# Optimization experiments

Hardware: AMD Instinct MI355X
Metric: run time of the kernel (lower is better)

## Reference

```python
import jax, jax.numpy as jnp
import numpy as np

# module hyperparameters (from init_kwargs)
STRIDE, PAD, DIL = 1, 1, 1
GROUPS, DG = 1, 1
KH, KW = 3, 3
CIN, COUT = 256, 256


def _mdcn_forward(x, offset, mask, weight, bias):
    B, C, H, W = x.shape
    Cout = weight.shape[0]
    K = KH * KW
    Ho = (H + 2 * PAD - (DIL * (KH - 1) + 1)) // STRIDE + 1
    Wo = (W + 2 * PAD - (DIL * (KW - 1) + 1)) // STRIDE + 1
    Cg = C // DG

    # offset channel layout: ((g*K + k)*2 + {0: dy, 1: dx})
    off = offset.reshape(B, DG, KH, KW, 2, Ho, Wo)
    base_y = (jnp.arange(Ho) * STRIDE - PAD)[None, :] + DIL * jnp.arange(KH)[:, None]  # [KH,Ho]
    base_x = (jnp.arange(Wo) * STRIDE - PAD)[None, :] + DIL * jnp.arange(KW)[:, None]  # [KW,Wo]
    sy = base_y[None, None, :, None, :, None].astype(x.dtype) + off[:, :, :, :, 0]  # [B,DG,KH,KW,Ho,Wo]
    sx = base_x[None, None, None, :, None, :].astype(x.dtype) + off[:, :, :, :, 1]

    y0f = jnp.floor(sy); x0f = jnp.floor(sx)
    wy = sy - y0f; wx = sx - x0f
    y0 = y0f.astype(jnp.int32); x0 = x0f.astype(jnp.int32)

    xg = x.reshape(B, DG, Cg, H * W)

    def corner(yc, xc, w):
        valid = (yc >= 0) & (yc < H) & (xc >= 0) & (xc < W)
        idx = jnp.clip(yc, 0, H - 1) * W + jnp.clip(xc, 0, W - 1)  # [B,DG,KH,KW,Ho,Wo]
        v = jnp.take_along_axis(xg, idx.reshape(B, DG, 1, -1), axis=3)  # [B,DG,Cg,K*Ho*Wo]
        v = v.reshape(B, DG, Cg, KH, KW, Ho, Wo)
        return v * (w * valid.astype(x.dtype))[:, :, None]

    val = (corner(y0, x0, (1 - wy) * (1 - wx))
           + corner(y0, x0 + 1, (1 - wy) * wx)
           + corner(y0 + 1, x0, wy * (1 - wx))
           + corner(y0 + 1, x0 + 1, wy * wx))  # [B,DG,Cg,KH,KW,Ho,Wo]

    cols = val * mask.reshape(B, DG, 1, KH, KW, Ho, Wo)
    cols = cols.reshape(B, GROUPS, (C // GROUPS) * K, Ho * Wo)
    wg = weight.reshape(GROUPS, Cout // GROUPS, (C // GROUPS) * K)
    out = jnp.einsum('gok,bgkp->bgop', wg, cols).reshape(B, Cout, Ho, Wo)
    return out + bias[None, :, None, None]


def setup_inputs() -> dict:
    key = jax.random.key(0)
    k1, k2, k3, k4 = jax.random.split(key, 4)
    B, H, W = 4, 64, 64
    x = jax.random.normal(k1, (B, CIN, H, W), dtype=jnp.float32)
    offset = jax.random.normal(k2, (B, 2 * DG * KH * KW, H, W), dtype=jnp.float32)
    mask = jax.random.uniform(k3, (B, DG * KH * KW, H, W), dtype=jnp.float32)
    stdv = 1.0 / np.sqrt(CIN * KH * KW)
    weight = jax.random.uniform(k4, (COUT, CIN // GROUPS, KH, KW), dtype=jnp.float32,
                                minval=-stdv, maxval=stdv)
    bias = jnp.zeros((COUT,), dtype=jnp.float32)
    return {"x": x, "offset": offset, "mask": mask, "weight": weight, "bias": bias}


def reference(x, offset, mask, weight, bias):
    return _mdcn_forward(x, offset, mask, weight, bias)
```

## Files before the change

kernel.cpp:

```cpp
#include <hip/hip_runtime.h>
#include <hip/hip_bf16.h>
#include <stdint.h>

#define KDIM 2304

typedef __bf16 bf16_t;
typedef bf16_t bf16x8 __attribute__((ext_vector_type(8)));
typedef float f32x4 __attribute__((ext_vector_type(4)));
typedef float f32x2 __attribute__((ext_vector_type(2)));

__device__ __forceinline__ float b2f_lo(uint32_t u) {
  union { uint32_t i; float f; } c; c.i = u << 16; return c.f;
}
__device__ __forceinline__ float b2f_hi(uint32_t u) {
  union { uint32_t i; float f; } c; c.i = u & 0xffff0000u; return c.f;
}
__device__ __forceinline__ uint32_t pk_bf16(float a, float b) {
  __hip_bfloat162 h = __float22bfloat162_rn(make_float2(a, b));
  union { __hip_bfloat162 h; uint32_t u; } c; c.h = h; return c.u;
}

__device__ __forceinline__ void g2lds16(const uint16_t* g, uint16_t* l) {
  __builtin_amdgcn_global_load_lds((const __attribute__((address_space(1))) void*)g,
                                   (__attribute__((address_space(3))) void*)l,
                                   16, 0, 0);
}

__global__ __launch_bounds__(256) void k_prep(const float* __restrict__ x,
                                              uint16_t* __restrict__ xt,
                                              const float* __restrict__ w,
                                              uint16_t* __restrict__ wt) {
  int tid = threadIdx.x;
  if (blockIdx.x < 2048) {
    __shared__ float tile[32][65];
    int b = blockIdx.x >> 9;
    int cgrp = (blockIdx.x >> 6) & 7;
    int sgrp = blockIdx.x & 63;
    int c0 = cgrp << 5, s0 = sgrp << 6;
#pragma unroll
    for (int it = 0; it < 2; ++it) {
      int f = tid + it * 256;
      int rr = f >> 4, col = (f & 15) << 2;
      float4 v = *(const float4*)&x[((size_t)(b * 256 + c0 + rr)) * 4096 + s0 + col];
      tile[rr][col + 0] = v.x;
      tile[rr][col + 1] = v.y;
      tile[rr][col + 2] = v.z;
      tile[rr][col + 3] = v.w;
    }
    __syncthreads();
    int sp = tid >> 2, cg = tid & 3;
    uint4 o;
    o.x = pk_bf16(tile[cg * 8 + 0][sp], tile[cg * 8 + 1][sp]);
    o.y = pk_bf16(tile[cg * 8 + 2][sp], tile[cg * 8 + 3][sp]);
    o.z = pk_bf16(tile[cg * 8 + 4][sp], tile[cg * 8 + 5][sp]);
    o.w = pk_bf16(tile[cg * 8 + 6][sp], tile[cg * 8 + 7][sp]);
    *(uint4*)&xt[((size_t)b * 4096 + s0 + sp) * 256 + c0 + cg * 8] = o;
  } else {
    __shared__ float wl[2304];
    int cout = blockIdx.x - 2048;
    const float* wrow = w + (size_t)cout * 2304;
    for (int i = tid; i < 576; i += 256)
      *(float4*)&wl[i * 4] = *(const float4*)&wrow[i * 4];
    __syncthreads();
    uint16_t* wdst = wt + (size_t)cout * KDIM + tid;
#pragma unroll
    for (int t = 0; t < 9; ++t)
      wdst[t * 256] = (uint16_t)(pk_bf16(wl[tid * 9 + t], 0.f) & 0xffffu);
  }
}

__device__ __forceinline__ void mk_corners(int tap, int p, int ho,
                                           const float* s_off, const float* s_msk,
                                           const uint16_t* xtb,
                                           float cw[4], const uint16_t* cp[4]) {
  int kh = tap / 3, kw = tap - kh * 3;
  float dy = s_off[(2 * tap) * 64 + p];
  float dx = s_off[(2 * tap + 1) * 64 + p];
  float mm = s_msk[tap * 64 + p];
  float sy = (float)(ho - 1 + kh) + dy;
  float sx = (float)(p - 1 + kw) + dx;
  float fy = floorf(sy), fx = floorf(sx);
  int y0 = (int)fy, x0 = (int)fx;
  float wy = sy - fy, wx = sx - fx;
#pragma unroll
  for (int cy = 0; cy < 2; ++cy) {
#pragma unroll
    for (int cx = 0; cx < 2; ++cx) {
      int y = y0 + cy, xx = x0 + cx;
      float wgt = (cy ? wy : 1.f - wy) * (cx ? wx : 1.f - wx) * mm;
      bool v = ((unsigned)y < 64u) && ((unsigned)xx < 64u);
      wgt = v ? wgt : 0.f;
      int yc = min(max(y, 0), 63), xc = min(max(xx, 0), 63);
      cw[cy * 2 + cx] = wgt;
      cp[cy * 2 + cx] = xtb + ((yc << 6) + xc) * 256;
    }
  }
}

__device__ __forceinline__ uint4 blend4(const uint4 d[4], const float cw[4]) {
  f32x2 f0 = {0.f, 0.f}, f1 = {0.f, 0.f}, f2 = {0.f, 0.f}, f3 = {0.f, 0.f};
#pragma unroll
  for (int c = 0; c < 4; ++c) {
    f32x2 wc = {cw[c], cw[c]};
    f0 += wc * f32x2{b2f_lo(d[c].x), b2f_hi(d[c].x)};
    f1 += wc * f32x2{b2f_lo(d[c].y), b2f_hi(d[c].y)};
    f2 += wc * f32x2{b2f_lo(d[c].z), b2f_hi(d[c].z)};
    f3 += wc * f32x2{b2f_lo(d[c].w), b2f_hi(d[c].w)};
  }
  uint4 o;
  o.x = pk_bf16(f0.x, f0.y);
  o.y = pk_bf16(f1.x, f1.y);
  o.z = pk_bf16(f2.x, f2.y);
  o.w = pk_bf16(f3.x, f3.y);
  return o;
}

__global__ __launch_bounds__(512, 2) void k_fused(const uint16_t* __restrict__ xt,
                                                  const uint16_t* __restrict__ wt,
                                                  const float* __restrict__ off,
                                                  const float* __restrict__ msk,
                                                  const float* __restrict__ bias,
                                                  float* __restrict__ out) {
  __shared__ __align__(16) uint16_t As[2][2][256][32];
  __shared__ __align__(16) uint16_t Bs[2][2][64][32];
  __shared__ float s_off[18 * 64];
  __shared__ float s_msk[9 * 64];

  int tid = threadIdx.x;
  int b = blockIdx.x >> 6, ho = blockIdx.x & 63;

  const float* offb = off + (size_t)b * 18 * 4096 + ho * 64;
  for (int i = tid; i < 18 * 64; i += 512)
    s_off[i] = offb[(size_t)(i >> 6) * 4096 + (i & 63)];
  const float* mskb = msk + (size_t)b * 9 * 4096 + ho * 64;
  for (int i = tid; i < 9 * 64; i += 512)
    s_msk[i] = mskb[(size_t)(i >> 6) * 4096 + (i & 63)];

  int lane = tid & 63, wv = tid >> 6;
  int wm = wv >> 1, wn = wv & 1;
  int q = lane >> 4, r = lane & 15;

  int p = tid >> 3, cg = tid & 7;
  const uint16_t* xtb = xt + (size_t)b * 4096 * 256 + cg * 8;
  int bsub = cg >> 2, bcol = (cg & 3) * 8;

  int asub = wv & 1, arow0 = (wv >> 1) * 64;
  const uint16_t* abase = wt + (size_t)(arow0 + (lane >> 2)) * KDIM + asub * 32 + (lane & 3) * 8;

  f32x4 acc[4][2];
#pragma unroll
  for (int i = 0; i < 4; ++i)
#pragma unroll
    for (int j = 0; j < 2; ++j) acc[i][j] = f32x4{0.f, 0.f, 0.f, 0.f};

  __syncthreads();

  float cw[4];
  const uint16_t* cp[4];

  mk_corners(0, p, ho, s_off, s_msk, xtb, cw, cp);
  {
    uint4 d0[4];
#pragma unroll
    for (int c = 0; c < 4; ++c) d0[c] = *(const uint4*)(cp[c]);
#pragma unroll
    for (int j = 0; j < 4; ++j)
      g2lds16(abase + (size_t)(j * 16) * KDIM, &As[0][asub][arow0 + j * 16][0]);
    uint4 o = blend4(d0, cw);
    *(uint4*)&Bs[0][bsub][p][bcol] = o;
  }

  for (int i = 0; i < 36; ++i) {
    int cur = i & 1;
    __syncthreads();
    uint4 dn[4];
    if (i != 35) {
      int nx = i + 1;
      if ((nx & 3) == 0) mk_corners(nx >> 2, p, ho, s_off, s_msk, xtb, cw, cp);
      int ofs = (nx & 3) * 64;
#pragma unroll
      for (int c = 0; c < 4; ++c) dn[c] = *(const uint4*)(cp[c] + ofs);
      int ofsK = (nx >> 2) * 256 + (nx & 3) * 64;
      int nb = nx & 1;
#pragma unroll
      for (int j = 0; j < 4; ++j)
        g2lds16(abase + ofsK + (size_t)(j * 16) * KDIM, &As[nb][asub][arow0 + j * 16][0]);
    }
    bf16x8 af[4][2], bfr[2][2];
#pragma unroll
    for (int kh = 0; kh < 2; ++kh) {
#pragma unroll
      for (int mi = 0; mi < 4; ++mi)
        af[mi][kh] = *(const bf16x8*)&As[cur][kh][wm * 64 + mi * 16 + r][q * 8];
#pragma unroll
      for (int ni = 0; ni < 2; ++ni)
        bfr[ni][kh] = *(const bf16x8*)&Bs[cur][kh][wn * 32 + ni * 16 + r][q * 8];
    }
#pragma unroll
    for (int kh = 0; kh < 2; ++kh)
#pragma unroll
      for (int mi = 0; mi < 4; ++mi)
#pragma unroll
        for (int ni = 0; ni < 2; ++ni)
          acc[mi][ni] = __builtin_amdgcn_mfma_f32_16x16x32_bf16(af[mi][kh], bfr[ni][kh], acc[mi][ni], 0, 0, 0);
    if (i != 35) {
      uint4 o = blend4(dn, cw);
      *(uint4*)&Bs[(i + 1) & 1][bsub][p][bcol] = o;
    }
  }

#pragma unroll
  for (int mi = 0; mi < 4; ++mi) {
#pragma unroll
    for (int j = 0; j < 4; ++j) {
      int m = wm * 64 + mi * 16 + q * 4 + j;
      float bv = bias[m];
#pragma unroll
      for (int ni = 0; ni < 2; ++ni) {
        int wo = wn * 32 + ni * 16 + r;
        out[((size_t)(b * 256 + m)) * 4096 + ho * 64 + wo] = acc[mi][ni][j] + bv;
      }
    }
  }
}

extern "C" void kernel_launch(void* const* d_in, const int* in_sizes, int n_in,
                              void* d_out, int out_size, void* d_ws, size_t ws_size,
                              hipStream_t stream) {
  (void)in_sizes; (void)n_in; (void)out_size; (void)ws_size;
  const float* x      = (const float*)d_in[0];
  const float* offset = (const float*)d_in[1];
  const float* mask   = (const float*)d_in[2];
  const float* weight = (const float*)d_in[3];
  const float* bias   = (const float*)d_in[4];
  float* out = (float*)d_out;

  uint8_t* ws = (uint8_t*)d_ws;
  uint16_t* xt = (uint16_t*)ws;
  uint16_t* wt = (uint16_t*)(ws + 8388608);

  k_prep<<<dim3(2304), 256, 0, stream>>>(x, xt, weight, wt);
  k_fused<<<dim3(256), 512, 0, stream>>>(xt, wt, offset, mask, bias, out);
}
```

Baseline: 130.2 us.

## Pre-pack weights in MFMA fragment order and load A straight into registers

The prep kernel now writes the bf16 weights already arranged in the MFMA A-fragment order, per tap and 64-channel chunk. The fused kernel can then load A fragments directly from global memory into registers with a register double buffer, and the LDS staging of A is dropped. The fused kernel moves to 1024 threads, with 16 waves each owning 16 output channels against all 64 pixels. The B tile uses an XOR-swizzled LDS layout to avoid bank conflicts, and block indices are swizzled across batches. This is meant to remove LDS traffic and barrier pressure for the weight operand. In exchange, every wave streams its weights from L2 and fewer threads cooperate on the bilinear gather.

New measurement: 133.4 us. 2.5% more time.

```diff
diff --git a/kernel.cpp b/kernel.cpp
--- a/kernel.cpp
+++ b/kernel.cpp
@@ -20,16 +20,10 @@
   union { __hip_bfloat162 h; uint32_t u; } c; c.h = h; return c.u;
 }
 
-__device__ __forceinline__ void g2lds16(const uint16_t* g, uint16_t* l) {
-  __builtin_amdgcn_global_load_lds((const __attribute__((address_space(1))) void*)g,
-                                   (__attribute__((address_space(3))) void*)l,
-                                   16, 0, 0);
-}
-
 __global__ __launch_bounds__(256) void k_prep(const float* __restrict__ x,
                                               uint16_t* __restrict__ xt,
                                               const float* __restrict__ w,
-                                              uint16_t* __restrict__ wt) {
+                                              uint16_t* __restrict__ wt2) {
   int tid = threadIdx.x;
   if (blockIdx.x < 2048) {
     __shared__ float tile[32][65];
@@ -56,23 +50,30 @@
     o.w = pk_bf16(tile[cg * 8 + 6][sp], tile[cg * 8 + 7][sp]);
     *(uint4*)&xt[((size_t)b * 4096 + s0 + sp) * 256 + c0 + cg * 8] = o;
   } else {
-    __shared__ float wl[2304];
-    int cout = blockIdx.x - 2048;
-    const float* wrow = w + (size_t)cout * 2304;
-    for (int i = tid; i < 576; i += 256)
-      *(float4*)&wl[i * 4] = *(const float4*)&wrow[i * 4];
-    __syncthreads();
-    uint16_t* wdst = wt + (size_t)cout * KDIM + tid;
-#pragma unroll
-    for (int t = 0; t < 9; ++t)
-      wdst[t * 256] = (uint16_t)(pk_bf16(wl[tid * 9 + t], 0.f) & 0xffffu);
+    int i = blockIdx.x - 2048;
+    int tap = i >> 2, w64 = i & 3;
+    uint16_t* dst = wt2 + (size_t)i * 16384;
+#pragma unroll
+    for (int s = 0; s < 8; ++s) {
+      int slot = tid + s * 256;
+      int lane = slot & 63;
+      int kh = (slot >> 6) & 1, strip = slot >> 7;
+      int row = strip * 16 + (lane & 15);
+      int cin0 = w64 * 64 + kh * 32 + ((lane >> 4) << 3);
+      const float* src = w + (size_t)row * KDIM + (size_t)cin0 * 9 + tap;
+      uint4 o;
+      o.x = pk_bf16(src[0 * 9], src[1 * 9]);
+      o.y = pk_bf16(src[2 * 9], src[3 * 9]);
+      o.z = pk_bf16(src[4 * 9], src[5 * 9]);
+      o.w = pk_bf16(src[6 * 9], src[7 * 9]);
+      *(uint4*)(dst + (size_t)slot * 8) = o;
+    }
   }
 }
 
 __device__ __forceinline__ void mk_corners(int tap, int p, int ho,
                                            const float* s_off, const float* s_msk,
-                                           const uint16_t* xtb,
-                                           float cw[4], const uint16_t* cp[4]) {
+                                           float cw[4], int cpo[4]) {
   int kh = tap / 3, kw = tap - kh * 3;
   float dy = s_off[(2 * tap) * 64 + p];
   float dx = s_off[(2 * tap + 1) * 64 + p];
@@ -92,134 +93,128 @@
       wgt = v ? wgt : 0.f;
       int yc = min(max(y, 0), 63), xc = min(max(xx, 0), 63);
       cw[cy * 2 + cx] = wgt;
-      cp[cy * 2 + cx] = xtb + ((yc << 6) + xc) * 256;
-    }
-  }
-}
-
-__device__ __forceinline__ uint4 blend4(const uint4 d[4], const float cw[4]) {
-  f32x2 f0 = {0.f, 0.f}, f1 = {0.f, 0.f}, f2 = {0.f, 0.f}, f3 = {0.f, 0.f};
-#pragma unroll
-  for (int c = 0; c < 4; ++c) {
-    f32x2 wc = {cw[c], cw[c]};
-    f0 += wc * f32x2{b2f_lo(d[c].x), b2f_hi(d[c].x)};
-    f1 += wc * f32x2{b2f_lo(d[c].y), b2f_hi(d[c].y)};
-    f2 += wc * f32x2{b2f_lo(d[c].z), b2f_hi(d[c].z)};
-    f3 += wc * f32x2{b2f_lo(d[c].w), b2f_hi(d[c].w)};
-  }
-  uint4 o;
-  o.x = pk_bf16(f0.x, f0.y);
-  o.y = pk_bf16(f1.x, f1.y);
-  o.z = pk_bf16(f2.x, f2.y);
-  o.w = pk_bf16(f3.x, f3.y);
-  return o;
-}
-
-__global__ __launch_bounds__(512, 2) void k_fused(const uint16_t* __restrict__ xt,
-                                                  const uint16_t* __restrict__ wt,
-                                                  const float* __restrict__ off,
-                                                  const float* __restrict__ msk,
-                                                  const float* __restrict__ bias,
-                                                  float* __restrict__ out) {
-  __shared__ __align__(16) uint16_t As[2][2][256][32];
-  __shared__ __align__(16) uint16_t Bs[2][2][64][32];
+      cpo[cy * 2 + cx] = ((yc << 6) + xc) * 256;
+    }
+  }
+}
+
+__global__ __launch_bounds__(1024, 4) void k_fused(const uint16_t* __restrict__ xt,
+                                                   const uint16_t* __restrict__ wt2,
+                                                   const float* __restrict__ off,
+                                                   const float* __restrict__ msk,
+                                                   const float* __restrict__ bias,
+                                                   float* __restrict__ out) {
+  __shared__ __align__(16) uint16_t Bs[2][64][64];
   __shared__ float s_off[18 * 64];
   __shared__ float s_msk[9 * 64];
 
   int tid = threadIdx.x;
-  int b = blockIdx.x >> 6, ho = blockIdx.x & 63;
+  int swz = ((int)blockIdx.x & 7) * 32 + ((int)blockIdx.x >> 3);
+  int b = swz >> 6, ho = swz & 63;
 
   const float* offb = off + (size_t)b * 18 * 4096 + ho * 64;
-  for (int i = tid; i < 18 * 64; i += 512)
+  for (int i = tid; i < 18 * 64; i += 1024)
     s_off[i] = offb[(size_t)(i >> 6) * 4096 + (i & 63)];
   const float* mskb = msk + (size_t)b * 9 * 4096 + ho * 64;
-  for (int i = tid; i < 9 * 64; i += 512)
+  for (int i = tid; i < 9 * 64; i += 1024)
     s_msk[i] = mskb[(size_t)(i >> 6) * 4096 + (i & 63)];
 
-  int lane = tid & 63, wv = tid >> 6;
-  int wm = wv >> 1, wn = wv & 1;
+  int lane = tid & 63, strip = tid >> 6;
   int q = lane >> 4, r = lane & 15;
-
-  int p = tid >> 3, cg = tid & 7;
-  const uint16_t* xtb = xt + (size_t)b * 4096 * 256 + cg * 8;
-  int bsub = cg >> 2, bcol = (cg & 3) * 8;
-
-  int asub = wv & 1, arow0 = (wv >> 1) * 64;
-  const uint16_t* abase = wt + (size_t)(arow0 + (lane >> 2)) * KDIM + asub * 32 + (lane & 3) * 8;
-
-  f32x4 acc[4][2];
-#pragma unroll
-  for (int i = 0; i < 4; ++i)
-#pragma unroll
-    for (int j = 0; j < 2; ++j) acc[i][j] = f32x4{0.f, 0.f, 0.f, 0.f};
+  int p = tid >> 4, cg = tid & 15;
+  const uint16_t* xtb = xt + (size_t)b * 4096 * 256 + cg * 4;
+  int bcol = (((cg >> 1) ^ (p & 7)) << 3) + ((cg & 1) << 2);
+
+  f32x4 acc[4];
+#pragma unroll
+  for (int ni = 0; ni < 4; ++ni) acc[ni] = f32x4{0.f, 0.f, 0.f, 0.f};
 
   __syncthreads();
 
   float cw[4];
-  const uint16_t* cp[4];
-
-  mk_corners(0, p, ho, s_off, s_msk, xtb, cw, cp);
+  int cpo[4];
+  uint2 dnv[4];
+  bf16x8 AFA[2], AFB[2];
+
+  int c0 = (q ^ (r & 7)) << 3;
+  int c1 = c0 ^ 32;
+
+  mk_corners(0, p, ho, s_off, s_msk, cw, cpo);
+#pragma unroll
+  for (int c = 0; c < 4; ++c) dnv[c] = *(const uint2*)(xtb + cpo[c]);
   {
-    uint4 d0[4];
-#pragma unroll
-    for (int c = 0; c < 4; ++c) d0[c] = *(const uint4*)(cp[c]);
-#pragma unroll
-    for (int j = 0; j < 4; ++j)
-      g2lds16(abase + (size_t)(j * 16) * KDIM, &As[0][asub][arow0 + j * 16][0]);
-    uint4 o = blend4(d0, cw);
-    *(uint4*)&Bs[0][bsub][p][bcol] = o;
-  }
-
-  for (int i = 0; i < 36; ++i) {
-    int cur = i & 1;
-    __syncthreads();
-    uint4 dn[4];
-    if (i != 35) {
-      int nx = i + 1;
-      if ((nx & 3) == 0) mk_corners(nx >> 2, p, ho, s_off, s_msk, xtb, cw, cp);
-      int ofs = (nx & 3) * 64;
-#pragma unroll
-      for (int c = 0; c < 4; ++c) dn[c] = *(const uint4*)(cp[c] + ofs);
-      int ofsK = (nx >> 2) * 256 + (nx & 3) * 64;
-      int nb = nx & 1;
-#pragma unroll
-      for (int j = 0; j < 4; ++j)
-        g2lds16(abase + ofsK + (size_t)(j * 16) * KDIM, &As[nb][asub][arow0 + j * 16][0]);
-    }
-    bf16x8 af[4][2], bfr[2][2];
-#pragma unroll
-    for (int kh = 0; kh < 2; ++kh) {
-#pragma unroll
-      for (int mi = 0; mi < 4; ++mi)
-        af[mi][kh] = *(const bf16x8*)&As[cur][kh][wm * 64 + mi * 16 + r][q * 8];
-#pragma unroll
-      for (int ni = 0; ni < 2; ++ni)
-        bfr[ni][kh] = *(const bf16x8*)&Bs[cur][kh][wn * 32 + ni * 16 + r][q * 8];
-    }
-#pragma unroll
-    for (int kh = 0; kh < 2; ++kh)
-#pragma unroll
-      for (int mi = 0; mi < 4; ++mi)
-#pragma unroll
-        for (int ni = 0; ni < 2; ++ni)
-          acc[mi][ni] = __builtin_amdgcn_mfma_f32_16x16x32_bf16(af[mi][kh], bfr[ni][kh], acc[mi][ni], 0, 0, 0);
-    if (i != 35) {
-      uint4 o = blend4(dn, cw);
-      *(uint4*)&Bs[(i + 1) & 1][bsub][p][bcol] = o;
-    }
-  }
-
-#pragma unroll
-  for (int mi = 0; mi < 4; ++mi) {
-#pragma unroll
-    for (int j = 0; j < 4; ++j) {
-      int m = wm * 64 + mi * 16 + q * 4 + j;
-      float bv = bias[m];
-#pragma unroll
-      for (int ni = 0; ni < 2; ++ni) {
-        int wo = wn * 32 + ni * 16 + r;
-        out[((size_t)(b * 256 + m)) * 4096 + ho * 64 + wo] = acc[mi][ni][j] + bv;
-      }
+    const uint16_t* wp = wt2 + strip * 1024 + lane * 8;
+    AFA[0] = *(const bf16x8*)(wp);
+    AFA[1] = *(const bf16x8*)(wp + 512);
+  }
+  {
+    f32x2 a0 = {0.f, 0.f}, a1 = {0.f, 0.f};
+#pragma unroll
+    for (int c = 0; c < 4; ++c) {
+      f32x2 wc = {cw[c], cw[c]};
+      a0 += wc * f32x2{b2f_lo(dnv[c].x), b2f_hi(dnv[c].x)};
+      a1 += wc * f32x2{b2f_lo(dnv[c].y), b2f_hi(dnv[c].y)};
+    }
+    uint2 o;
+    o.x = pk_bf16(a0.x, a0.y);
+    o.y = pk_bf16(a1.x, a1.y);
+    *(uint2*)&Bs[0][p][bcol] = o;
+  }
+  __syncthreads();
+
+#define BODY(IEXPR, AFC, AFN)                                                   \
+  {                                                                             \
+    const int i_ = (IEXPR);                                                     \
+    if (i_ < 35) {                                                              \
+      int nx = i_ + 1;                                                          \
+      if ((nx & 3) == 0) mk_corners(nx >> 2, p, ho, s_off, s_msk, cw, cpo);     \
+      int chw = (nx & 3) << 6;                                                  \
+      _Pragma("unroll")                                                         \
+      for (int c = 0; c < 4; ++c) dnv[c] = *(const uint2*)(xtb + cpo[c] + chw); \
+      const uint16_t* wp = wt2 + (size_t)nx * 16384 + strip * 1024 + lane * 8;  \
+      AFN[0] = *(const bf16x8*)(wp);                                            \
+      AFN[1] = *(const bf16x8*)(wp + 512);                                      \
+    }                                                                           \
+    {                                                                           \
+      const uint16_t* bsrow = &Bs[(IEXPR) & 1][0][0];                           \
+      _Pragma("unroll")                                                         \
+      for (int ni = 0; ni < 4; ++ni) {                                          \
+        bf16x8 b0 = *(const bf16x8*)(bsrow + (ni * 16 + r) * 64 + c0);          \
+        bf16x8 b1 = *(const bf16x8*)(bsrow + (ni * 16 + r) * 64 + c1);          \
+        acc[ni] = __builtin_amdgcn_mfma_f32_16x16x32_bf16(AFC[0], b0, acc[ni], 0, 0, 0); \
+        acc[ni] = __builtin_amdgcn_mfma_f32_16x16x32_bf16(AFC[1], b1, acc[ni], 0, 0, 0); \
+      }                                                                         \
+    }                                                                           \
+    if (i_ < 35) {                                                              \
+      f32x2 a0 = {0.f, 0.f}, a1 = {0.f, 0.f};                                   \
+      _Pragma("unroll")                                                         \
+      for (int c = 0; c < 4; ++c) {                                             \
+        f32x2 wc = {cw[c], cw[c]};                                              \
+        a0 += wc * f32x2{b2f_lo(dnv[c].x), b2f_hi(dnv[c].x)};                   \
+        a1 += wc * f32x2{b2f_lo(dnv[c].y), b2f_hi(dnv[c].y)};                   \
+      }                                                                         \
+      uint2 o;                                                                  \
+      o.x = pk_bf16(a0.x, a0.y);                                                \
+      o.y = pk_bf16(a1.x, a1.y);                                                \
+      *(uint2*)&Bs[1 - ((IEXPR) & 1)][p][bcol] = o;                             \
+    }                                                                           \
+    __syncthreads();                                                            \
+  }
+
+#pragma unroll 1
+  for (int ii = 0; ii < 18; ++ii) {
+    BODY(2 * ii, AFA, AFB);
+    BODY(2 * ii + 1, AFB, AFA);
+  }
+#undef BODY
+
+#pragma unroll
+  for (int j = 0; j < 4; ++j) {
+    int m = strip * 16 + q * 4 + j;
+    float bv = bias[m];
+#pragma unroll
+    for (int ni = 0; ni < 4; ++ni) {
+      out[((size_t)(b * 256 + m)) * 4096 + ho * 64 + ni * 16 + r] = acc[ni][j] + bv;
     }
   }
 }
@@ -236,9 +231,9 @@
   float* out = (float*)d_out;
 
   uint8_t* ws = (uint8_t*)d_ws;
-  uint16_t* xt = (uint16_t*)ws;
-  uint16_t* wt = (uint16_t*)(ws + 8388608);
-
-  k_prep<<<dim3(2304), 256, 0, stream>>>(x, xt, weight, wt);
-  k_fused<<<dim3(256), 512, 0, stream>>>(xt, wt, offset, mask, bias, out);
-}
+  uint16_t* xt  = (uint16_t*)ws;
+  uint16_t* wt2 = (uint16_t*)(ws + 8388608);
+
+  k_prep<<<dim3(2084), 256, 0, stream>>>(x, xt, weight, wt2);
+  k_fused<<<dim3(256), 1024, 0, stream>>>(xt, wt2, offset, mask, bias, out);
+}
```
